# Kernel tuning notes

Hardware: AMD Instinct MI355X
Metric: run time of the kernel (lower is better)

The kernel has to match this reference:

```python
import jax, jax.numpy as jnp
import numpy as np

D_MODEL = 1024
N_HEADS = 16
D_HEAD = D_MODEL // N_HEADS
D_FF = 4096
BATCH = 2
SEQ = 2048
LN_EPS = 1e-5


def setup_inputs() -> dict:
    key = jax.random.key(0)
    ks = jax.random.split(key, 12)
    s = 1.0 / np.sqrt(D_MODEL)
    x = jax.random.normal(ks[0], (BATCH, SEQ, D_MODEL), dtype=jnp.float32)
    mask = jnp.broadcast_to(jnp.tril(jnp.ones((SEQ, SEQ), jnp.int32)), (BATCH, SEQ, SEQ))
    return {
        "x": x,
        "mask": mask,
        # per-head projections stacked: [H, D, Dh] (bias=False in source)
        "Wq": jax.random.normal(ks[1], (N_HEADS, D_MODEL, D_HEAD), jnp.float32) * s,
        "Wk": jax.random.normal(ks[2], (N_HEADS, D_MODEL, D_HEAD), jnp.float32) * s,
        "Wv": jax.random.normal(ks[3], (N_HEADS, D_MODEL, D_HEAD), jnp.float32) * s,
        "Wo": jax.random.normal(ks[4], (D_MODEL, D_MODEL), jnp.float32) * s,
        "ln1_w": jnp.ones((D_MODEL,), jnp.float32),
        "ln1_b": jnp.zeros((D_MODEL,), jnp.float32),
        "ln2_w": jnp.ones((D_MODEL,), jnp.float32),
        "ln2_b": jnp.zeros((D_MODEL,), jnp.float32),
        "W1": jax.random.normal(ks[5], (D_MODEL, D_FF), jnp.float32) * s,
        "b1": jnp.zeros((D_FF,), jnp.float32),
        "W2": jax.random.normal(ks[6], (D_FF, D_MODEL), jnp.float32) * (1.0 / np.sqrt(D_FF)),
        "b2": jnp.zeros((D_MODEL,), jnp.float32),
    }


def layer_norm(x, w, b):
    mu = jnp.mean(x, axis=-1, keepdims=True)
    var = jnp.var(x, axis=-1, keepdims=True)
    return (x - mu) * jax.lax.rsqrt(var + LN_EPS) * w + b


def reference(x, mask, Wq, Wk, Wv, Wo, ln1_w, ln1_b, ln2_w, ln2_b, W1, b1, W2, b2):
    # pre-LN masked self-attention
    h = layer_norm(x, ln1_w, ln1_b)
    q = jnp.einsum("bsd,hde->bhse", h, Wq)  # [B,H,S,Dh]
    k = jnp.einsum("bsd,hde->bhse", h, Wk)
    v = jnp.einsum("bsd,hde->bhse", h, Wv)
    scores = jnp.einsum("bhse,bhte->bhst", q, k) / np.sqrt(D_HEAD)
    scores = jnp.where(mask[:, None, :, :].astype(bool), scores, -jnp.inf)
    weights = jax.nn.softmax(scores, axis=-1)
    attn = jnp.einsum("bhst,bhte->bhse", weights, v)  # [B,H,S,Dh]
    # concat heads (head order = last-dim order in torch.cat)
    concat = attn.transpose(0, 2, 1, 3).reshape(x.shape[0], x.shape[1], D_MODEL)
    att_out = concat @ Wo
    att_x = x + att_out
    # FFN with exact (erf) GELU, matching nn.GELU default
    h2 = layer_norm(att_x, ln2_w, ln2_b)
    ff = jax.nn.gelu(h2 @ W1 + b1, approximate=False) @ W2 + b2
    return att_x + ff
```

## Files before the change

kernel.cpp:

```cpp
#include <hip/hip_runtime.h>
#include <hip/hip_bf16.h>
#include <math.h>

#define D_MODEL 1024
#define N_HEADS 16
#define D_HEAD  64
#define D_FF    4096
#define BATCH   2
#define SEQ     2048
#define NTOK    (BATCH*SEQ)

typedef __hip_bfloat16 bf16;
typedef __attribute__((ext_vector_type(8))) short short8;
typedef __attribute__((ext_vector_type(4))) float floatx4;

template<typename TIN>
__global__ void ln_kernel(const TIN* __restrict__ x,
                          const float* __restrict__ w,
                          const float* __restrict__ b,
                          bf16* __restrict__ out) {
    int row = blockIdx.x;
    int tid = threadIdx.x;
    const long base = (long)row * D_MODEL;
    float v[4];
    float s = 0.f, sq = 0.f;
#pragma unroll
    for (int i = 0; i < 4; ++i) {
        float xv = (float)x[base + tid + i*256];
        v[i] = xv; s += xv; sq += xv*xv;
    }
    __shared__ float r1[256], r2[256];
    r1[tid] = s; r2[tid] = sq; __syncthreads();
    for (int off = 128; off > 0; off >>= 1) {
        if (tid < off) { r1[tid] += r1[tid+off]; r2[tid] += r2[tid+off]; }
        __syncthreads();
    }
    float mean = r1[0] * (1.f/D_MODEL);
    float var  = r2[0] * (1.f/D_MODEL) - mean*mean;
    float rstd = rsqrtf(var + 1e-5f);
#pragma unroll
    for (int i = 0; i < 4; ++i) {
        int c = tid + i*256;
        out[base + c] = __float2bfloat16((v[i] - mean) * rstd * w[c] + b[c]);
    }
}

__global__ __launch_bounds__(256) void wcvt_kernel(const float* __restrict__ W,
                                                   bf16* __restrict__ Wt,
                                                   int K, int N) {
    __shared__ float t[32][33];
    int n0 = blockIdx.x * 32, k0 = blockIdx.y * 32;
    int lx = threadIdx.x & 31, ly = threadIdx.x >> 5;
#pragma unroll
    for (int i = 0; i < 4; ++i) {
        int k = ly + i * 8;
        t[k][lx] = W[(long)(k0 + k) * N + n0 + lx];
    }
    __syncthreads();
#pragma unroll
    for (int i = 0; i < 4; ++i) {
        int n = ly + i * 8;
        Wt[(long)(n0 + n) * K + k0 + lx] = __float2bfloat16(t[lx][n]);
    }
}

__global__ __launch_bounds__(256) void wcvt_qkv(const float* __restrict__ Wq,
                                                const float* __restrict__ Wk,
                                                const float* __restrict__ Wv,
                                                bf16* __restrict__ outp) {
    __shared__ float t[32][33];
    int z = blockIdx.z, mat = z >> 4, head = z & 15;
    const float* W = (mat == 0 ? Wq : mat == 1 ? Wk : Wv) + (long)head * D_MODEL * D_HEAD;
    bf16* Wt = outp + (long)z * D_HEAD * D_MODEL;
    int n0 = blockIdx.x * 32, k0 = blockIdx.y * 32;
    int lx = threadIdx.x & 31, ly = threadIdx.x >> 5;
#pragma unroll
    for (int i = 0; i < 4; ++i) {
        int k = ly + i * 8;
        t[k][lx] = W[(long)(k0 + k) * D_HEAD + n0 + lx];
    }
    __syncthreads();
#pragma unroll
    for (int i = 0; i < 4; ++i) {
        int n = ly + i * 8;
        Wt[(long)(n0 + n) * D_MODEL + k0 + lx] = __float2bfloat16(t[lx][n]);
    }
}

template<int ROWS>
__device__ inline void stage_tile(const bf16* g, int gstride, short* lds) {
    int lane = threadIdx.x & 63, wave = threadIdx.x >> 6;
#pragma unroll
    for (int it = 0; it < ROWS / 64; ++it) {
        int c = wave + it * 4;
        const bf16* gp = g + (long)(c * 16 + (lane >> 2)) * gstride + (lane & 3) * 8;
        short* lp = lds + c * 512 + lane * 8;
        __builtin_amdgcn_global_load_lds(
            (const __attribute__((address_space(1))) void*)gp,
            (__attribute__((address_space(3))) void*)lp, 16, 0, 0);
    }
}

template<int BM, int BN, int BIAS, int ACT, int RES, int OUTBF16>
__device__ inline void gemm_bf_body(const bf16* __restrict__ A, int lda,
                                    const bf16* __restrict__ Wt, int K,
                                    const float* __restrict__ bias,
                                    const float* __restrict__ resid,
                                    void* __restrict__ Cout, int ldc,
                                    int row0, int col0, short* As, short* Bs) {
    constexpr int MI = BM / 32;
    constexpr int NR = BN / 32;
    int tid  = threadIdx.x;
    int wave = tid >> 6, lane = tid & 63;
    int quad = lane >> 4, l16 = lane & 15;
    int wm = (wave >> 1) * (BM / 2);
    int wn = (wave & 1) * (BN / 2);

    floatx4 acc[MI][NR];
#pragma unroll
    for (int mi = 0; mi < MI; ++mi)
#pragma unroll
        for (int ni = 0; ni < NR; ++ni)
            acc[mi][ni] = (floatx4){0.f, 0.f, 0.f, 0.f};

    for (int k0 = 0; k0 < K; k0 += 64) {
        stage_tile<BM>(A  + (long)row0 * lda + k0,      lda, As);
        stage_tile<BM>(A  + (long)row0 * lda + k0 + 32, lda, As + BM * 32);
        stage_tile<BN>(Wt + (long)col0 * K   + k0,      K,   Bs);
        stage_tile<BN>(Wt + (long)col0 * K   + k0 + 32, K,   Bs + BN * 32);
        __syncthreads();

#pragma unroll
        for (int p = 0; p < 2; ++p) {
            const short* Ap = As + p * BM * 32;
            const short* Bp = Bs + p * BN * 32;
            short8 af[MI], bfr[NR];
#pragma unroll
            for (int mi = 0; mi < MI; ++mi)
                af[mi] = *(const short8*)&Ap[(wm + mi * 16 + l16) * 32 + quad * 8];
#pragma unroll
            for (int ni = 0; ni < NR; ++ni)
                bfr[ni] = *(const short8*)&Bp[(wn + ni * 16 + l16) * 32 + quad * 8];
#pragma unroll
            for (int mi = 0; mi < MI; ++mi)
#pragma unroll
                for (int ni = 0; ni < NR; ++ni)
                    acc[mi][ni] = __builtin_amdgcn_mfma_f32_16x16x32_bf16(
                        af[mi], bfr[ni], acc[mi][ni], 0, 0, 0);
        }
        __syncthreads();
    }

#pragma unroll
    for (int mi = 0; mi < MI; ++mi) {
#pragma unroll
        for (int ni = 0; ni < NR; ++ni) {
#pragma unroll
            for (int r = 0; r < 4; ++r) {
                int row = row0 + wm + mi * 16 + quad * 4 + r;
                int col = col0 + wn + ni * 16 + l16;
                float v = acc[mi][ni][r];
                if (BIAS) v += bias[col];
                if (ACT == 1) v = 0.5f * v * (1.f + erff(v * 0.70710678118654752f));
                long idx = (long)row * ldc + col;
                if (RES == 1) v += resid[idx];
                if (OUTBF16) ((bf16*)Cout)[idx] = __float2bfloat16(v);
                else         ((float*)Cout)[idx] = v;
            }
        }
    }
}

template<int BM, int BN, int BIAS, int ACT, int RES, int OUTBF16>
__global__ __launch_bounds__(256) void mfma_gemm_bf(
    const bf16* __restrict__ A, int lda,
    const bf16* __restrict__ Wt, int K,
    const float* __restrict__ bias, const float* __restrict__ resid,
    void* __restrict__ Cout, int ldc)
{
    __shared__ short As[BM * 64];
    __shared__ short Bs[BN * 64];
    gemm_bf_body<BM, BN, BIAS, ACT, RES, OUTBF16>(
        A, lda, Wt, K, bias, resid, Cout, ldc,
        blockIdx.y * BM, blockIdx.x * BN, As, Bs);
}

struct QkvOut { bf16* o[3]; };
__global__ __launch_bounds__(256) void qkv_kernel(const bf16* __restrict__ h1,
                                                  const bf16* __restrict__ wqkv,
                                                  QkvOut a) {
    int z = blockIdx.z;
    int bh = z / 3, mat = z - bh * 3;
    int b = bh >> 4, head = bh & 15;
    const bf16* Ab = h1 + (long)b * SEQ * D_MODEL;
    const bf16* Wt = wqkv + (long)(mat * 16 + head) * D_HEAD * D_MODEL;
    bf16* Cb = a.o[mat] + (long)bh * SEQ * D_HEAD;
    __shared__ short As[128 * 64];
    __shared__ short Bs[64 * 64];
    gemm_bf_body<128, 64, 0, 0, 0, 1>(
        Ab, D_MODEL, Wt, D_MODEL, nullptr, nullptr, Cb, D_HEAD,
        blockIdx.y * 128, 0, As, Bs);
}

__global__ __launch_bounds__(256) void fattn_mfma(const bf16* __restrict__ q,
                                                  const bf16* __restrict__ k,
                                                  const bf16* __restrict__ v,
                                                  bf16* __restrict__ concat) {
    int byr = blockIdx.y;
    int tile = (byr < 8) ? byr : 23 - byr;
    int bh = blockIdx.x;
    int b  = bh >> 4, h = bh & 15;
    int tid = threadIdx.x;
    int wave = tid >> 6, lane = tid & 63;
    int quad = lane >> 4, l16 = lane & 15;
    const long base = (long)bh * SEQ * D_HEAD;
    const int r0g = tile * 128;

    __shared__ short Ks[64 * 72];
    __shared__ short Vt[64 * 72];
    __shared__ short Ps[4][32 * 72];

    short8 qf[2][2];
#pragma unroll
    for (int rb = 0; rb < 2; ++rb) {
        const short* qrow = (const short*)(q + base +
            (long)(r0g + wave * 32 + rb * 16 + l16) * D_HEAD);
        qf[rb][0] = *(const short8*)(qrow + quad * 8);
        qf[rb][1] = *(const short8*)(qrow + 32 + quad * 8);
#pragma unroll
        for (int c = 0; c < 2; ++c)
#pragma unroll
            for (int j = 0; j < 8; ++j) {
                float f = __uint_as_float(((unsigned)(unsigned short)qf[rb][c][j]) << 16)
                          * 0.18033688f;
                qf[rb][c][j] = __builtin_bit_cast(short, __float2bfloat16(f));
            }
    }

    short8 onesf;
    {
        short o1 = (l16 == 0) ? (short)0x3F80 : (short)0;
#pragma unroll
        for (int j = 0; j < 8; ++j) onesf[j] = o1;
    }

    floatx4 o[2][4];
#pragma unroll
    for (int rb = 0; rb < 2; ++rb)
#pragma unroll
        for (int nb = 0; nb < 4; ++nb) o[rb][nb] = (floatx4){0.f, 0.f, 0.f, 0.f};
    floatx4 l4[2] = {(floatx4){0.f,0.f,0.f,0.f}, (floatx4){0.f,0.f,0.f,0.f}};

    const int ktmax = 2 * tile + 1;
    for (int kt = 0; kt <= ktmax; ++kt) {
        __syncthreads();
        {
            int t = tid >> 2, c = tid & 3;
            const short* krow = (const short*)(k + base + (long)(kt * 64 + t) * D_HEAD);
            *(uint4*)&Ks[t * 72 + c * 16]     = *(const uint4*)(krow + c * 16);
            *(uint4*)&Ks[t * 72 + c * 16 + 8] = *(const uint4*)(krow + c * 16 + 8);
        }
        {
            int tp = (tid & 31) * 2;
            int d0 = ((tid >> 5) & 7) * 8;
            const short* v0 = (const short*)(v + base + (long)(kt * 64 + tp) * D_HEAD + d0);
            short va[8], vb[8];
            *(uint4*)va = *(const uint4*)v0;
            *(uint4*)vb = *(const uint4*)(v0 + D_HEAD);
#pragma unroll
            for (int j = 0; j < 8; ++j) {
                unsigned pk = (unsigned)(unsigned short)va[j] |
                              ((unsigned)(unsigned short)vb[j] << 16);
                *(unsigned*)&Vt[(d0 + j) * 72 + tp] = pk;
            }
        }
        __syncthreads();

        if (kt * 64 > r0g + wave * 32 + 31) continue;

        floatx4 s[2][4];
#pragma unroll
        for (int nb = 0; nb < 4; ++nb) {
            short8 kf0 = *(const short8*)&Ks[(nb * 16 + l16) * 72 + quad * 8];
            short8 kf1 = *(const short8*)&Ks[(nb * 16 + l16) * 72 + 32 + quad * 8];
#pragma unroll
            for (int rb = 0; rb < 2; ++rb) {
                floatx4 z4 = (floatx4){0.f, 0.f, 0.f, 0.f};
                z4 = __builtin_amdgcn_mfma_f32_16x16x32_bf16(qf[rb][0], kf0, z4, 0, 0, 0);
                z4 = __builtin_amdgcn_mfma_f32_16x16x32_bf16(qf[rb][1], kf1, z4, 0, 0, 0);
                s[rb][nb] = z4;
            }
        }

        if (kt >= 2 * tile) {
#pragma unroll
            for (int rb = 0; rb < 2; ++rb) {
                int qg = r0g + wave * 32 + rb * 16 + quad * 4;
#pragma unroll
                for (int nb = 0; nb < 4; ++nb) {
                    int kg = kt * 64 + nb * 16 + l16;
#pragma unroll
                    for (int r = 0; r < 4; ++r)
                        if (kg > qg + r) s[rb][nb][r] = -1e30f;
                }
            }
        }

        short* Pw = &Ps[wave][0];
#pragma unroll
        for (int rb = 0; rb < 2; ++rb)
#pragma unroll
            for (int nb = 0; nb < 4; ++nb)
#pragma unroll
                for (int r = 0; r < 4; ++r) {
                    float p = exp2f(s[rb][nb][r]);
                    Pw[(rb * 16 + quad * 4 + r) * 72 + nb * 16 + l16] =
                        __builtin_bit_cast(short, __float2bfloat16(p));
                }

        short8 pf[2][2];
#pragma unroll
        for (int rb = 0; rb < 2; ++rb) {
            pf[rb][0] = *(const short8*)&Pw[(rb * 16 + l16) * 72 + quad * 8];
            pf[rb][1] = *(const short8*)&Pw[(rb * 16 + l16) * 72 + 32 + quad * 8];
        }
#pragma unroll
        for (int nb = 0; nb < 4; ++nb) {
            short8 vf0 = *(const short8*)&Vt[(nb * 16 + l16) * 72 + quad * 8];
            short8 vf1 = *(const short8*)&Vt[(nb * 16 + l16) * 72 + 32 + quad * 8];
#pragma unroll
            for (int rb = 0; rb < 2; ++rb) {
                o[rb][nb] = __builtin_amdgcn_mfma_f32_16x16x32_bf16(pf[rb][0], vf0, o[rb][nb], 0, 0, 0);
                o[rb][nb] = __builtin_amdgcn_mfma_f32_16x16x32_bf16(pf[rb][1], vf1, o[rb][nb], 0, 0, 0);
            }
        }
#pragma unroll
        for (int rb = 0; rb < 2; ++rb) {
            l4[rb] = __builtin_amdgcn_mfma_f32_16x16x32_bf16(pf[rb][0], onesf, l4[rb], 0, 0, 0);
            l4[rb] = __builtin_amdgcn_mfma_f32_16x16x32_bf16(pf[rb][1], onesf, l4[rb], 0, 0, 0);
        }
    }

#pragma unroll
    for (int rb = 0; rb < 2; ++rb) {
        float linv[4];
#pragma unroll
        for (int r = 0; r < 4; ++r) {
            float lv = __shfl(l4[rb][r], lane & 48);
            linv[r] = 1.f / lv;
        }
#pragma unroll
        for (int nb = 0; nb < 4; ++nb)
#pragma unroll
            for (int r = 0; r < 4; ++r) {
                int row = r0g + wave * 32 + rb * 16 + quad * 4 + r;
                int col = h * D_HEAD + nb * 16 + l16;
                concat[(long)(b * SEQ + row) * D_MODEL + col] =
                    __float2bfloat16(o[rb][nb][r] * linv[r]);
            }
    }
}

extern "C" void kernel_launch(void* const* d_in, const int* in_sizes, int n_in,
                              void* d_out, int out_size, void* d_ws, size_t ws_size,
                              hipStream_t stream) {
    const float* x    = (const float*)d_in[0];
    const float* Wq   = (const float*)d_in[2];
    const float* Wk   = (const float*)d_in[3];
    const float* Wv   = (const float*)d_in[4];
    const float* Wo   = (const float*)d_in[5];
    const float* ln1w = (const float*)d_in[6];
    const float* ln1b = (const float*)d_in[7];
    const float* ln2w = (const float*)d_in[8];
    const float* ln2b = (const float*)d_in[9];
    const float* W1   = (const float*)d_in[10];
    const float* b1   = (const float*)d_in[11];
    const float* W2   = (const float*)d_in[12];
    const float* b2   = (const float*)d_in[13];
    float* out = (float*)d_out;

    char* wsb = (char*)d_ws;
    const size_t MB = 1024*1024;
    bf16*  h1      = (bf16*)(wsb + 0*MB);
    bf16*  qb      = (bf16*)(wsb + 8*MB);
    bf16*  kb      = (bf16*)(wsb + 16*MB);
    bf16*  vb      = (bf16*)(wsb + 24*MB);
    bf16*  wqkv_bf = (bf16*)(wsb + 32*MB);
    bf16*  cc      = (bf16*)(wsb + 0*MB);
    bf16*  wo_bf   = (bf16*)(wsb + 8*MB);
    bf16*  w1_bf   = (bf16*)(wsb + 10*MB);
    bf16*  h2      = (bf16*)(wsb + 0*MB);
    bf16*  ff      = (bf16*)(wsb + 24*MB);
    bf16*  w2_bf   = (bf16*)(wsb + 8*MB);

    ln_kernel<float><<<NTOK, 256, 0, stream>>>(x, ln1w, ln1b, h1);

    wcvt_qkv<<<dim3(2, 32, 48), 256, 0, stream>>>(Wq, Wk, Wv, wqkv_bf);

    QkvOut qa; qa.o[0] = qb; qa.o[1] = kb; qa.o[2] = vb;
    qkv_kernel<<<dim3(1, 16, 96), 256, 0, stream>>>(h1, wqkv_bf, qa);

    fattn_mfma<<<dim3(BATCH*N_HEADS, SEQ/128), 256, 0, stream>>>(qb, kb, vb, cc);

    wcvt_kernel<<<dim3(D_MODEL/32, D_MODEL/32), 256, 0, stream>>>(Wo, wo_bf, D_MODEL, D_MODEL);
    wcvt_kernel<<<dim3(D_FF/32,    D_MODEL/32), 256, 0, stream>>>(W1, w1_bf, D_MODEL, D_FF);

    mfma_gemm_bf<64,128,0,0,1,0><<<dim3(8,64), 256, 0, stream>>>(
        cc, D_MODEL, wo_bf, D_MODEL, nullptr, x, out, D_MODEL);

    ln_kernel<float><<<NTOK, 256, 0, stream>>>(out, ln2w, ln2b, h2);

    mfma_gemm_bf<128,128,1,1,0,1><<<dim3(32,32), 256, 0, stream>>>(
        h2, D_MODEL, w1_bf, D_MODEL, b1, nullptr, ff, D_FF);

    wcvt_kernel<<<dim3(D_MODEL/32, D_FF/32), 256, 0, stream>>>(W2, w2_bf, D_FF, D_MODEL);

    mfma_gemm_bf<64,128,1,0,1,0><<<dim3(8,64), 256, 0, stream>>>(
        ff, D_FF, w2_bf, D_FF, b2, out, out, D_MODEL);
}
```

Baseline: 403.2 us.

## Fuse QKV into one wide GEMM, merge weight casts, use fast GELU

```diff
diff --git a/kernel.cpp b/kernel.cpp
--- a/kernel.cpp
+++ b/kernel.cpp
@@ -64,6 +64,30 @@
     }
 }
 
+__global__ __launch_bounds__(256) void wcvt_wo_w1(const float* __restrict__ Wo,
+                                                  const float* __restrict__ W1,
+                                                  bf16* __restrict__ wo_bf,
+                                                  bf16* __restrict__ w1_bf) {
+    __shared__ float t[32][33];
+    int gx = blockIdx.x;
+    const float* W; bf16* Wt; int N, n0;
+    if (gx < 32) { W = Wo; Wt = wo_bf; N = D_MODEL; n0 = gx * 32; }
+    else         { W = W1; Wt = w1_bf; N = D_FF;    n0 = (gx - 32) * 32; }
+    int k0 = blockIdx.y * 32;
+    int lx = threadIdx.x & 31, ly = threadIdx.x >> 5;
+#pragma unroll
+    for (int i = 0; i < 4; ++i) {
+        int k = ly + i * 8;
+        t[k][lx] = W[(long)(k0 + k) * N + n0 + lx];
+    }
+    __syncthreads();
+#pragma unroll
+    for (int i = 0; i < 4; ++i) {
+        int n = ly + i * 8;
+        Wt[(long)(n0 + n) * D_MODEL + k0 + lx] = __float2bfloat16(t[lx][n]);
+    }
+}
+
 __global__ __launch_bounds__(256) void wcvt_qkv(const float* __restrict__ Wq,
                                                 const float* __restrict__ Wk,
                                                 const float* __restrict__ Wv,
@@ -101,13 +125,11 @@
     }
 }
 
-template<int BM, int BN, int BIAS, int ACT, int RES, int OUTBF16>
-__device__ inline void gemm_bf_body(const bf16* __restrict__ A, int lda,
-                                    const bf16* __restrict__ Wt, int K,
-                                    const float* __restrict__ bias,
-                                    const float* __restrict__ resid,
-                                    void* __restrict__ Cout, int ldc,
-                                    int row0, int col0, short* As, short* Bs) {
+template<int BM, int BN>
+__device__ inline void gemm_accum(const bf16* __restrict__ A, int lda,
+                                  const bf16* __restrict__ Wt, int K,
+                                  int row0, int col0, short* As, short* Bs,
+                                  floatx4 (&acc)[BM/32][BN/32]) {
     constexpr int MI = BM / 32;
     constexpr int NR = BN / 32;
     int tid  = threadIdx.x;
@@ -116,13 +138,6 @@
     int wm = (wave >> 1) * (BM / 2);
     int wn = (wave & 1) * (BN / 2);
 
-    floatx4 acc[MI][NR];
-#pragma unroll
-    for (int mi = 0; mi < MI; ++mi)
-#pragma unroll
-        for (int ni = 0; ni < NR; ++ni)
-            acc[mi][ni] = (floatx4){0.f, 0.f, 0.f, 0.f};
-
     for (int k0 = 0; k0 < K; k0 += 64) {
         stage_tile<BM>(A  + (long)row0 * lda + k0,      lda, As);
         stage_tile<BM>(A  + (long)row0 * lda + k0 + 32, lda, As + BM * 32);
@@ -149,25 +164,6 @@
                         af[mi], bfr[ni], acc[mi][ni], 0, 0, 0);
         }
         __syncthreads();
-    }
-
-#pragma unroll
-    for (int mi = 0; mi < MI; ++mi) {
-#pragma unroll
-        for (int ni = 0; ni < NR; ++ni) {
-#pragma unroll
-            for (int r = 0; r < 4; ++r) {
-                int row = row0 + wm + mi * 16 + quad * 4 + r;
-                int col = col0 + wn + ni * 16 + l16;
-                float v = acc[mi][ni][r];
-                if (BIAS) v += bias[col];
-                if (ACT == 1) v = 0.5f * v * (1.f + erff(v * 0.70710678118654752f));
-                long idx = (long)row * ldc + col;
-                if (RES == 1) v += resid[idx];
-                if (OUTBF16) ((bf16*)Cout)[idx] = __float2bfloat16(v);
-                else         ((float*)Cout)[idx] = v;
-            }
-        }
     }
 }
 
@@ -178,28 +174,85 @@
     const float* __restrict__ bias, const float* __restrict__ resid,
     void* __restrict__ Cout, int ldc)
 {
+    constexpr int MI = BM / 32;
+    constexpr int NR = BN / 32;
     __shared__ short As[BM * 64];
     __shared__ short Bs[BN * 64];
-    gemm_bf_body<BM, BN, BIAS, ACT, RES, OUTBF16>(
-        A, lda, Wt, K, bias, resid, Cout, ldc,
-        blockIdx.y * BM, blockIdx.x * BN, As, Bs);
+    int row0 = blockIdx.y * BM, col0 = blockIdx.x * BN;
+    int tid = threadIdx.x, wave = tid >> 6, lane = tid & 63;
+    int quad = lane >> 4, l16 = lane & 15;
+    int wm = (wave >> 1) * (BM / 2);
+    int wn = (wave & 1) * (BN / 2);
+
+    floatx4 acc[MI][NR];
+#pragma unroll
+    for (int mi = 0; mi < MI; ++mi)
+#pragma unroll
+        for (int ni = 0; ni < NR; ++ni)
+            acc[mi][ni] = (floatx4){0.f, 0.f, 0.f, 0.f};
+
+    gemm_accum<BM, BN>(A, lda, Wt, K, row0, col0, As, Bs, acc);
+
+#pragma unroll
+    for (int mi = 0; mi < MI; ++mi) {
+#pragma unroll
+        for (int ni = 0; ni < NR; ++ni) {
+#pragma unroll
+            for (int r = 0; r < 4; ++r) {
+                int row = row0 + wm + mi * 16 + quad * 4 + r;
+                int col = col0 + wn + ni * 16 + l16;
+                float v = acc[mi][ni][r];
+                if (BIAS) v += bias[col];
+                if (ACT == 1) {
+                    float x2 = v * v;
+                    float arg = fminf(v * fmaf(0.1029392f, x2, 2.3021182f), 20.f);
+                    float t = exp2f(arg);
+                    v = v * t * __builtin_amdgcn_rcpf(t + 1.f);
+                }
+                long idx = (long)row * ldc + col;
+                if (RES == 1) v += resid[idx];
+                if (OUTBF16) ((bf16*)Cout)[idx] = __float2bfloat16(v);
+                else         ((float*)Cout)[idx] = v;
+            }
+        }
+    }
 }
 
 struct QkvOut { bf16* o[3]; };
 __global__ __launch_bounds__(256) void qkv_kernel(const bf16* __restrict__ h1,
                                                   const bf16* __restrict__ wqkv,
                                                   QkvOut a) {
-    int z = blockIdx.z;
-    int bh = z / 3, mat = z - bh * 3;
-    int b = bh >> 4, head = bh & 15;
-    const bf16* Ab = h1 + (long)b * SEQ * D_MODEL;
-    const bf16* Wt = wqkv + (long)(mat * 16 + head) * D_HEAD * D_MODEL;
-    bf16* Cb = a.o[mat] + (long)bh * SEQ * D_HEAD;
     __shared__ short As[128 * 64];
-    __shared__ short Bs[64 * 64];
-    gemm_bf_body<128, 64, 0, 0, 0, 1>(
-        Ab, D_MODEL, Wt, D_MODEL, nullptr, nullptr, Cb, D_HEAD,
-        blockIdx.y * 128, 0, As, Bs);
+    __shared__ short Bs[128 * 64];
+    int row0 = blockIdx.y * 128, col0 = blockIdx.x * 128;
+    int tid = threadIdx.x, wave = tid >> 6, lane = tid & 63;
+    int quad = lane >> 4, l16 = lane & 15;
+    int wm = (wave >> 1) * 64, wn = (wave & 1) * 64;
+
+    floatx4 acc[4][4];
+#pragma unroll
+    for (int mi = 0; mi < 4; ++mi)
+#pragma unroll
+        for (int ni = 0; ni < 4; ++ni)
+            acc[mi][ni] = (floatx4){0.f, 0.f, 0.f, 0.f};
+
+    gemm_accum<128, 128>(h1, D_MODEL, wqkv, D_MODEL, row0, col0, As, Bs, acc);
+
+#pragma unroll
+    for (int mi = 0; mi < 4; ++mi) {
+#pragma unroll
+        for (int ni = 0; ni < 4; ++ni) {
+#pragma unroll
+            for (int r = 0; r < 4; ++r) {
+                int row = row0 + wm + mi * 16 + quad * 4 + r;
+                int c   = col0 + wn + ni * 16 + l16;
+                int mat = c >> 10, hd = (c >> 6) & 15, d = c & 63;
+                int b = row >> 11, s = row & 2047;
+                a.o[mat][(((long)(b * 16 + hd) * SEQ + s) << 6) + d] =
+                    __float2bfloat16(acc[mi][ni][r]);
+            }
+        }
+    }
 }
 
 __global__ __launch_bounds__(256) void fattn_mfma(const bf16* __restrict__ q,
@@ -398,12 +451,11 @@
     wcvt_qkv<<<dim3(2, 32, 48), 256, 0, stream>>>(Wq, Wk, Wv, wqkv_bf);
 
     QkvOut qa; qa.o[0] = qb; qa.o[1] = kb; qa.o[2] = vb;
-    qkv_kernel<<<dim3(1, 16, 96), 256, 0, stream>>>(h1, wqkv_bf, qa);
+    qkv_kernel<<<dim3(24, 32), 256, 0, stream>>>(h1, wqkv_bf, qa);
 
     fattn_mfma<<<dim3(BATCH*N_HEADS, SEQ/128), 256, 0, stream>>>(qb, kb, vb, cc);
 
-    wcvt_kernel<<<dim3(D_MODEL/32, D_MODEL/32), 256, 0, stream>>>(Wo, wo_bf, D_MODEL, D_MODEL);
-    wcvt_kernel<<<dim3(D_FF/32,    D_MODEL/32), 256, 0, stream>>>(W1, w1_bf, D_MODEL, D_FF);
+    wcvt_wo_w1<<<dim3(160, 32), 256, 0, stream>>>(Wo, W1, wo_bf, w1_bf);
 
     mfma_gemm_bf<64,128,0,0,1,0><<<dim3(8,64), 256, 0, stream>>>(
         cc, D_MODEL, wo_bf, D_MODEL, nullptr, x, out, D_MODEL);
```

Result: faster. 384.8 us (-4.6%).
